# Performance work log

Hardware: AMD Instinct MI355X
Metric: run time of the kernel (lower is better)

## Reference

```python
import jax, jax.numpy as jnp
import numpy as np

EPS_BN = 1e-5
EPS_COS = 1e-8

N, F_IN, HID, OUT, S, NNZ = 50000, 1024, 256, 280, 5000, 800000


def setup_inputs() -> dict:
    key = jax.random.key(0)
    ks = jax.random.split(key, 20)
    inp = {}
    inp["x"] = jax.random.normal(ks[0], (N, F_IN), jnp.float32)
    inp["y"] = jax.random.normal(ks[1], (S, OUT), jnp.float32)
    inp["adj_rows"] = jax.random.randint(ks[2], (NNZ,), 0, N, jnp.int32)
    inp["adj_cols"] = jax.random.randint(ks[3], (NNZ,), 0, N, jnp.int32)
    inp["adj_vals"] = jax.random.uniform(ks[4], (NNZ,), jnp.float32)
    inp["agg_rows"] = jax.random.randint(ks[5], (N,), 0, S, jnp.int32)
    inp["agg_vals"] = jax.random.uniform(ks[6], (N,), jnp.float32)
    inp["perm"] = jax.random.permutation(ks[7], N).astype(jnp.int32)
    # parameters (kaiming-ish scale)
    def lin(k, fi, fo):
        k1, k2 = jax.random.split(k)
        w = jax.random.normal(k1, (fi, fo), jnp.float32) / np.sqrt(fi)
        b = jax.random.normal(k2, (fo,), jnp.float32) * 0.01
        return w, b
    inp["mlp_W"], inp["mlp_b"] = lin(ks[8], F_IN, HID)
    inp["bn_gamma"] = jnp.ones((HID,), jnp.float32)
    inp["bn_beta"] = jnp.zeros((HID,), jnp.float32)
    inp["hg_W1"], inp["hg_b1"] = lin(ks[9], HID, HID)
    inp["hg_W2"], inp["hg_b2"] = lin(ks[10], HID, HID)
    inp["hg_prelu"] = jnp.float32(0.25)
    inp["pred_W"], inp["pred_b"] = lin(ks[11], HID, OUT)
    inp["dgi_W"], inp["dgi_b"] = lin(ks[12], HID, OUT)
    inp["dgi_prelu"] = jnp.float32(0.25)
    return inp


def _spmm(rows, cols, vals, M, n_out):
    # sparse(H) @ M : gather source rows, scale by edge value, scatter-add to dest
    return jax.ops.segment_sum(vals[:, None] * M[cols], rows, num_segments=n_out)


def _prelu(t, a):
    return jnp.where(t >= 0, t, a * t)


def _leaky(t, s):
    return jnp.where(t >= 0, t, s * t)


def reference(x, y, adj_rows, adj_cols, adj_vals, agg_rows, agg_vals, perm,
              mlp_W, mlp_b, bn_gamma, bn_beta, hg_W1, hg_b1, hg_W2, hg_b2,
              hg_prelu, pred_W, pred_b, dgi_W, dgi_b, dgi_prelu):
    n = x.shape[0]
    s = y.shape[0]
    # mlp: Linear -> LeakyReLU(0.1) -> BatchNorm1d (batch stats, training mode)
    h0 = _leaky(x @ mlp_W + mlp_b, 0.1)
    mu = jnp.mean(h0, axis=0)
    var = jnp.mean((h0 - mu) ** 2, axis=0)  # biased, as torch BN training
    h0 = bn_gamma * (h0 - mu) * jax.lax.rsqrt(var + EPS_BN) + bn_beta
    # HGNN, num_layers=2 (dropout = identity in eval)
    t = _spmm(adj_rows, adj_cols, adj_vals, h0 @ hg_W1 + hg_b1, n)
    t = _prelu(t, hg_prelu)
    t = _spmm(adj_rows, adj_cols, adj_vals, t @ hg_W2 + hg_b2, n)
    h = _leaky(t, 0.01)
    x_prime = _leaky(h @ pred_W + pred_b, 0.01)
    # Xenium: loss = MSE(agg_mtx @ x_prime, y); agg_mtx has one nnz per cell
    agg = jax.ops.segment_sum(agg_vals[:, None] * x_prime, agg_rows, num_segments=s)
    loss = jnp.mean((agg - y) ** 2)
    # DGI (1-layer HGNN with PReLU)
    h1 = _prelu(_spmm(adj_rows, adj_cols, adj_vals, h0 @ dgi_W + dgi_b, n), dgi_prelu)
    c = jnp.mean(h1, axis=0)  # (OUT,)
    h2 = _prelu(_spmm(adj_rows, adj_cols, adj_vals, h0[perm] @ dgi_W + dgi_b, n), dgi_prelu)
    c_norm = jnp.linalg.norm(c)
    def cos(hm):
        return (hm @ c) / jnp.maximum(jnp.linalg.norm(hm, axis=1) * c_norm, EPS_COS)
    loss = loss + jnp.mean(1.0 - cos(h1)) + jnp.mean(jnp.maximum(cos(h2), 0.0))
    return (loss, x_prime)
```

## Files before the change

kernel.cpp:

```cpp
#include <hip/hip_runtime.h>
#include <hip/hip_bf16.h>

#define DEVI __device__ __forceinline__

typedef __attribute__((ext_vector_type(8))) short short8;
typedef __attribute__((ext_vector_type(4))) float float4v;

DEVI float bf2f(__hip_bfloat16 v) { return __bfloat162float(v); }
DEVI float ldbs(const ushort* p, size_t i) { return bf2f(((const __hip_bfloat16*)p)[i]); }
DEVI ushort f2bs(float v) {
    __hip_bfloat16 h = __float2bfloat16(v);
    return *(ushort*)&h;
}
DEVI float bfs2f(short s) {
    ushort u = (ushort)s;
    return bf2f(*(__hip_bfloat16*)&u);
}

DEVI float ldin(const void* p, size_t i, int isf32) {
    return isf32 ? ((const float*)p)[i] : bf2f(((const __hip_bfloat16*)p)[i]);
}
DEVI void stio(void* p, size_t i, float v, int isf32) {
    if (isf32) ((float*)p)[i] = v;
    else ((ushort*)p)[i] = f2bs(v);
}

template <int ACT>
DEVI float act_fn(float v, float alpha) {
    if (ACT == 1) return v >= 0.f ? v : 0.1f * v;
    if (ACT == 2) return v >= 0.f ? v : 0.01f * v;
    if (ACT == 3) return v >= 0.f ? v : alpha * v;
    return v;
}

DEVI float waveRed(float v) {
#pragma unroll
    for (int o = 32; o > 0; o >>= 1) v += __shfl_down(v, o);
    return v;
}

DEVI float blockRed(float v) {
    __shared__ float sm[16];
    int lane = threadIdx.x & 63, w = threadIdx.x >> 6;
    v = waveRed(v);
    if (lane == 0) sm[w] = v;
    __syncthreads();
    if (w == 0) {
        int nw = (blockDim.x + 63) >> 6;
        v = (lane < nw) ? sm[lane] : 0.f;
        v = waveRed(v);
    }
    return v;
}

__global__ void probe_k(const void* __restrict__ x, int* __restrict__ flag) {
    __shared__ int sfails;
    int t = threadIdx.x;
    if (t == 0) sfails = 0;
    __syncthreads();
    const __hip_bfloat16* xb = (const __hip_bfloat16*)x;
    int my = 0;
    for (int i = t; i < 4096; i += 256) {
        float v = bf2f(xb[i]);
        float a = fabsf(v);
        if (!(a <= 64.f) || (v != 0.f && a < 1e-6f)) my++;
    }
    atomicAdd(&sfails, my);
    __syncthreads();
    if (t == 0) flag[0] = (sfails > 409) ? 1 : 0;
}

struct Cvt5 {
    const void* src[5];
    ushort* dst[5];
    int K[5];
    int N[5];
};
__global__ void cvt_all_k(Cvt5 d, const int* __restrict__ flagp) {
    int f32 = flagp[0];
    int seg = blockIdx.y;
    int idx = blockIdx.x * blockDim.x + threadIdx.x;
    int K = d.K[seg], Nc = d.N[seg];
    int total = K * Nc;
    if (idx < total) {
        int k = idx / Nc, n = idx % Nc;
        d.dst[seg][(size_t)n * K + k] = f2bs(ldin(d.src[seg], idx, f32));
    }
}

#define TP 40
template <int AMODE, int ACT, int OMODE, int BMODE>
__global__ __launch_bounds__(256) void mgemm_k(
    const void* __restrict__ A, const ushort* __restrict__ Bt,
    const void* __restrict__ bias, const float* __restrict__ rsc,
    const void* __restrict__ alpha_p, void* __restrict__ outp, ushort* __restrict__ outp2,
    const int* __restrict__ flagp, int M, int K, int Nc, int LDo) {
    __shared__ short As[128 * TP];
    __shared__ short Bs[128 * TP];
    const int f32 = flagp[0];
    const int tid = threadIdx.x;
    const int lane = tid & 63;
    const int l15 = lane & 15;
    const int quad = lane >> 4;
    const int wid = tid >> 6;
    const int mW = (wid >> 1) * 64;
    const int nW = (wid & 1) * 64;
    const int mBase = blockIdx.y * 128;
    const int nBase = blockIdx.x * 128;

    float4v acc[4][4];
#pragma unroll
    for (int i = 0; i < 4; i++)
#pragma unroll
        for (int j = 0; j < 4; j++) acc[i][j] = (float4v){0.f, 0.f, 0.f, 0.f};

    short8 sa[2], sb[2];
    float4v fa[2][2];

    auto issue_tile = [&](int k0) {
#pragma unroll
        for (int i = 0; i < 2; i++) {
            int chunk = i * 256 + tid;
            int row = chunk >> 2;
            int c = chunk & 3;
            int gr = mBase + row;
            int gn = nBase + row;
            size_t geA = (size_t)gr * K + k0 + c * 8;
            if (AMODE == 0 && f32) {
                if (gr < M) {
                    const float* af = (const float*)A + geA;
                    fa[i][0] = *(const float4v*)af;
                    fa[i][1] = *(const float4v*)(af + 4);
                } else {
                    fa[i][0] = (float4v){0.f, 0.f, 0.f, 0.f};
                    fa[i][1] = (float4v){0.f, 0.f, 0.f, 0.f};
                }
            } else {
                sa[i] = (gr < M) ? *(const short8*)((const ushort*)A + geA)
                                 : (short8){0, 0, 0, 0, 0, 0, 0, 0};
            }
            sb[i] = (gn < Nc) ? *(const short8*)(Bt + (size_t)gn * K + k0 + c * 8)
                              : (short8){0, 0, 0, 0, 0, 0, 0, 0};
        }
    };

    auto commit_tile = [&]() {
#pragma unroll
        for (int i = 0; i < 2; i++) {
            int chunk = i * 256 + tid;
            int row = chunk >> 2;
            int c = chunk & 3;
            short8 va;
            if (AMODE == 0 && f32) {
#pragma unroll
                for (int j = 0; j < 4; j++) va[j] = (short)f2bs(fa[i][0][j]);
#pragma unroll
                for (int j = 0; j < 4; j++) va[4 + j] = (short)f2bs(fa[i][1][j]);
            } else {
                va = sa[i];
            }
            *(short8*)&As[row * TP + c * 8] = va;
            *(short8*)&Bs[row * TP + c * 8] = sb[i];
        }
    };

    const int nk = K >> 5;
    issue_tile(0);
    for (int t = 0; t < nk; ++t) {
        __syncthreads();
        commit_tile();
        if (t + 1 < nk) issue_tile((t + 1) << 5);
        __syncthreads();

        short8 af[4], bf[4];
#pragma unroll
        for (int i = 0; i < 4; i++)
            af[i] = *(const short8*)&As[(mW + i * 16 + l15) * TP + quad * 8];
#pragma unroll
        for (int j = 0; j < 4; j++)
            bf[j] = *(const short8*)&Bs[(nW + j * 16 + l15) * TP + quad * 8];
#pragma unroll
        for (int i = 0; i < 4; i++)
#pragma unroll
            for (int j = 0; j < 4; j++)
                acc[i][j] =
                    __builtin_amdgcn_mfma_f32_16x16x32_bf16(af[i], bf[j], acc[i][j], 0, 0, 0);
    }

    const float alpha = (ACT == 3) ? ldin(alpha_p, 0, f32) : 0.f;
#pragma unroll
    for (int i = 0; i < 4; i++) {
#pragma unroll
        for (int j = 0; j < 4; j++) {
            int gcn = nBase + nW + j * 16 + l15;
            if (gcn >= Nc) continue;
            float bv = ldin(bias, gcn, f32);
#pragma unroll
            for (int r = 0; r < 4; r++) {
                int grm = mBase + mW + i * 16 + quad * 4 + r;
                if (grm >= M) continue;
                float be = (BMODE == 1) ? rsc[grm] * bv : bv;
                float v = act_fn<ACT>(acc[i][j][r] + be, alpha);
                if (OMODE == 1) {
                    stio(outp, 1 + (size_t)grm * Nc + gcn, v, f32);
                    outp2[(size_t)grm * LDo + gcn] = f2bs(v);
                } else {
                    ((ushort*)outp)[(size_t)grm * LDo + gcn] = f2bs(v);
                }
            }
        }
    }
}

__global__ void count_k(const int* __restrict__ rows, int* __restrict__ counts, int nnz) {
    int i = blockIdx.x * blockDim.x + threadIdx.x;
    if (i < nnz) atomicAdd(&counts[rows[i]], 1);
}

__global__ __launch_bounds__(1024) void scan_local_k(const int* __restrict__ counts,
                                                     int* __restrict__ offs,
                                                     int* __restrict__ bsums, int n) {
    __shared__ int sm[1024];
    int t = threadIdx.x;
    int g = blockIdx.x * 1024 + t;
    int v = (g < n) ? counts[g] : 0;
    sm[t] = v;
    __syncthreads();
    for (int d = 1; d < 1024; d <<= 1) {
        int add = (t >= d) ? sm[t - d] : 0;
        __syncthreads();
        sm[t] += add;
        __syncthreads();
    }
    if (g < n) offs[g] = sm[t] - v;
    if (t == 1023) bsums[blockIdx.x] = sm[t];
}

__global__ void scan_bsums_k(int* bsums, int nb) {
    if (threadIdx.x == 0 && blockIdx.x == 0) {
        int acc = 0;
        for (int i = 0; i < nb; i++) {
            int v = bsums[i];
            bsums[i] = acc;
            acc += v;
        }
    }
}

__global__ void scan_add_k(int* __restrict__ offs, const int* __restrict__ bsums, int n, int nnz) {
    int g = blockIdx.x * blockDim.x + threadIdx.x;
    if (g < n) offs[g] += bsums[g >> 10];
    if (g == 0) offs[n] = nnz;
}

__global__ void fill_k(const int* __restrict__ rows, const int* __restrict__ cols,
                       const void* __restrict__ vals, const int* __restrict__ perm,
                       const int* __restrict__ offs, int* __restrict__ cursor,
                       int* __restrict__ cols_s, int* __restrict__ colsp_s,
                       float* __restrict__ vals_s, float* __restrict__ rsum,
                       const int* __restrict__ flagp, int nnz) {
    int e = blockIdx.x * blockDim.x + threadIdx.x;
    if (e < nnz) {
        int r = rows[e];
        int pos = offs[r] + atomicAdd(&cursor[r], 1);
        int c = cols[e];
        float v = ldin(vals, e, flagp[0]);
        cols_s[pos] = c;
        colsp_s[pos] = perm[c];
        vals_s[pos] = v;
        atomicAdd(&rsum[r], v);
    }
}

__global__ void fill_s_k(const int* __restrict__ rows, const void* __restrict__ vals,
                         const int* __restrict__ offs, int* __restrict__ cursor,
                         int* __restrict__ idx_s, float* __restrict__ val_s,
                         const int* __restrict__ flagp, int n) {
    int e = blockIdx.x * blockDim.x + threadIdx.x;
    if (e < n) {
        int r = rows[e];
        int pos = offs[r] + atomicAdd(&cursor[r], 1);
        idx_s[pos] = e;
        val_s[pos] = ldin(vals, e, flagp[0]);
    }
}

template <int ACT, bool DUAL>
__global__ __launch_bounds__(256) void spmms_k(
    const int* __restrict__ offs, const int* __restrict__ cols_s,
    const int* __restrict__ colsp_s, const float* __restrict__ vals_s,
    const void* __restrict__ alpha_p, const int* __restrict__ flagp,
    const ushort* __restrict__ Min, ushort* __restrict__ out1, ushort* __restrict__ out2,
    int Nrow, int LD) {
    int bid = blockIdx.x;
    int slice = bid & 7;
    int row = (bid >> 3) * 4 + (threadIdx.x >> 6);
    if (row >= Nrow) return;
    int lane = threadIdx.x & 63;
    int e = lane >> 2, ch = lane & 3;
    int sbase = slice * 32 + ch * 8;
    float alpha = (ACT == 3) ? ldin(alpha_p, 0, flagp[0]) : 0.f;
    int s = offs[row], en = offs[row + 1];
    float a[8] = {}, b[8] = {};
    for (int i = s + e; i < en; i += 16) {
        int c = cols_s[i];
        float v = vals_s[i];
        short8 h = *(const short8*)(Min + (size_t)c * LD + sbase);
#pragma unroll
        for (int j = 0; j < 8; j++) a[j] += v * bfs2f(h[j]);
        if (DUAL) {
            int cp = colsp_s[i];
            short8 g = *(const short8*)(Min + (size_t)cp * LD + sbase);
#pragma unroll
            for (int j = 0; j < 8; j++) b[j] += v * bfs2f(g[j]);
        }
    }
#pragma unroll
    for (int m = 4; m < 64; m <<= 1) {
#pragma unroll
        for (int j = 0; j < 8; j++) {
            a[j] += __shfl_xor(a[j], m);
            if (DUAL) b[j] += __shfl_xor(b[j], m);
        }
    }
    if (e == 0) {
        short8 o;
        size_t obase = (size_t)row * LD + sbase;
#pragma unroll
        for (int j = 0; j < 8; j++) o[j] = (short)f2bs(act_fn<ACT>(a[j], alpha));
        *(short8*)(out1 + obase) = o;
        if (DUAL) {
#pragma unroll
            for (int j = 0; j < 8; j++) o[j] = (short)f2bs(act_fn<ACT>(b[j], alpha));
            *(short8*)(out2 + obase) = o;
        }
    }
}

__global__ __launch_bounds__(256) void aggmse_k(
    const int* __restrict__ soffs, const int* __restrict__ sidx, const float* __restrict__ sval,
    const ushort* __restrict__ xp, const void* __restrict__ y, const int* __restrict__ flagp,
    float* __restrict__ lacc, int S, int F, int LDxp) {
    int srow = blockIdx.x * 4 + (threadIdx.x >> 6);
    int lane = threadIdx.x & 63;
    int half = lane >> 5, l5 = lane & 31;
    int FC = F >> 3;
    bool has1 = (l5 + 32) < FC;
    float a0[8] = {}, a1[8] = {};
    if (srow < S) {
        int s = soffs[srow], e = soffs[srow + 1];
        constexpr int DEPTH = 4;
        int i = s + half;
        for (; i + 2 * (DEPTH - 1) < e; i += 2 * DEPTH) {
            int n[DEPTH];
            float v[DEPTH];
#pragma unroll
            for (int u = 0; u < DEPTH; u++) {
                n[u] = sidx[i + 2 * u];
                v[u] = sval[i + 2 * u];
            }
            short8 h0v[DEPTH], h1v[DEPTH];
#pragma unroll
            for (int u = 0; u < DEPTH; u++) {
                const ushort* src = xp + (size_t)n[u] * LDxp;
                h0v[u] = *(const short8*)(src + l5 * 8);
                if (has1) h1v[u] = *(const short8*)(src + (l5 + 32) * 8);
            }
#pragma unroll
            for (int u = 0; u < DEPTH; u++) {
#pragma unroll
                for (int j = 0; j < 8; j++) a0[j] += v[u] * bfs2f(h0v[u][j]);
                if (has1) {
#pragma unroll
                    for (int j = 0; j < 8; j++) a1[j] += v[u] * bfs2f(h1v[u][j]);
                }
            }
        }
        for (; i < e; i += 2) {
            float v = sval[i];
            int n = sidx[i];
            const ushort* src = xp + (size_t)n * LDxp;
            short8 h = *(const short8*)(src + l5 * 8);
#pragma unroll
            for (int j = 0; j < 8; j++) a0[j] += v * bfs2f(h[j]);
            if (has1) {
                short8 h2 = *(const short8*)(src + (l5 + 32) * 8);
#pragma unroll
                for (int j = 0; j < 8; j++) a1[j] += v * bfs2f(h2[j]);
            }
        }
    }
#pragma unroll
    for (int j = 0; j < 8; j++) {
        a0[j] += __shfl_xor(a0[j], 32);
        if (has1) a1[j] += __shfl_xor(a1[j], 32);
    }
    float ss = 0.f;
    if (srow < S && half == 0) {
        int f32 = flagp[0];
        size_t base = (size_t)srow * F;
#pragma unroll
        for (int j = 0; j < 8; j++) {
            float d = a0[j] - ldin(y, base + l5 * 8 + j, f32);
            ss += d * d;
        }
        if (has1) {
#pragma unroll
            for (int j = 0; j < 8; j++) {
                float d = a1[j] - ldin(y, base + (l5 + 32) * 8 + j, f32);
                ss += d * d;
            }
        }
    }
    ss = blockRed(ss);
    if (threadIdx.x == 0) atomicAdd(&lacc[0], ss);
}

__global__ __launch_bounds__(256) void bn_stats_k(const ushort* __restrict__ h,
                                                  float* __restrict__ sum,
                                                  float* __restrict__ sumsq, int nrows, int rpb) {
    int c = threadIdx.x;
    int rs = blockIdx.x * rpb;
    int re = min(rs + rpb, nrows);
    float s = 0.f, s2 = 0.f;
    int H = blockDim.x;
    for (int r = rs; r < re; r++) {
        float v = ldbs(h, (size_t)r * H + c);
        s += v;
        s2 += v * v;
    }
    atomicAdd(&sum[c], s);
    atomicAdd(&sumsq[c], s2);
}

__global__ void bn_final_k(const float* __restrict__ sum, const float* __restrict__ sumsq,
                           const void* __restrict__ gamma, const void* __restrict__ beta,
                           float* __restrict__ scale, float* __restrict__ shift,
                           const int* __restrict__ flagp, int nrows) {
    int c = threadIdx.x;
    int f32 = flagp[0];
    float mu = sum[c] / nrows;
    float var = sumsq[c] / nrows - mu * mu;
    float sc = ldin(gamma, c, f32) * rsqrtf(var + 1e-5f);
    scale[c] = sc;
    shift[c] = ldin(beta, c, f32) - mu * sc;
}

__global__ __launch_bounds__(256) void bn_apply_k(ushort* __restrict__ h,
                                                  const float* __restrict__ scale,
                                                  const float* __restrict__ shift, int total8,
                                                  int H) {
    int idx = blockIdx.x * 256 + threadIdx.x;
    if (idx >= total8) return;
    size_t base = (size_t)idx * 8;
    int c = (int)(base % H);
    short8 v = *(short8*)(h + base);
    short8 o;
#pragma unroll
    for (int j = 0; j < 8; j++) o[j] = (short)f2bs(bfs2f(v[j]) * scale[c + j] + shift[c + j]);
    *(short8*)(h + base) = o;
}

__global__ __launch_bounds__(320) void colsum_k(const ushort* __restrict__ h,
                                                float* __restrict__ accum, int nrows, int F,
                                                int rpb) {
    int f = threadIdx.x;
    if (f >= F) return;
    int rs = blockIdx.x * rpb;
    int re = min(rs + rpb, nrows);
    float s = 0.f;
    for (int r = rs; r < re; r++) s += ldbs(h, (size_t)r * F + f);
    atomicAdd(&accum[f], s);
}

__global__ __launch_bounds__(320) void cfinal_k(const float* __restrict__ accum,
                                                float* __restrict__ c, float* __restrict__ cnorm,
                                                int N, int F) {
    int f = threadIdx.x;
    float v = 0.f;
    if (f < F) {
        v = accum[f] / N;
        c[f] = v;
    }
    float s2 = blockRed(v * v);
    if (threadIdx.x == 0) cnorm[0] = sqrtf(s2);
}

template <int MODE>
__global__ __launch_bounds__(256) void cos_k(const ushort* __restrict__ h,
                                             const float* __restrict__ c,
                                             const float* __restrict__ cnorm,
                                             float* __restrict__ acc, int N, int F) {
    int gw = (blockIdx.x * blockDim.x + threadIdx.x) >> 6;
    int lane = threadIdx.x & 63;
    int nw = (gridDim.x * blockDim.x) >> 6;
    float cn = cnorm[0];
    float s = 0.f;
    for (int row = gw; row < N; row += nw) {
        float dot = 0.f, nsq = 0.f;
        for (int f = lane; f < F; f += 64) {
            float v = ldbs(h, (size_t)row * F + f);
            dot += v * c[f];
            nsq += v * v;
        }
#pragma unroll
        for (int o = 32; o > 0; o >>= 1) {
            dot += __shfl_down(dot, o);
            nsq += __shfl_down(nsq, o);
        }
        if (lane == 0) {
            float cosv = dot / fmaxf(sqrtf(nsq) * cn, 1e-8f);
            s += (MODE == 1) ? fmaxf(cosv, 0.f) : cosv;
        }
    }
    s = blockRed(s);
    if (threadIdx.x == 0) atomicAdd(acc, s);
}

__global__ void final_k(const float* __restrict__ lacc, void* __restrict__ dout,
                        const int* __restrict__ flagp, int SOUT, int N) {
    if (threadIdx.x == 0 && blockIdx.x == 0) {
        float loss = lacc[0] / SOUT + (1.f - lacc[1] / N) + lacc[2] / N;
        stio(dout, 0, loss, flagp[0]);
    }
}

extern "C" void kernel_launch(void* const* d_in, const int* in_sizes, int n_in,
                              void* d_out, int out_size, void* d_ws, size_t ws_size,
                              hipStream_t stream) {
    const void* x = d_in[0];
    const void* y = d_in[1];
    const int* adj_rows = (const int*)d_in[2];
    const int* adj_cols = (const int*)d_in[3];
    const void* adj_vals = d_in[4];
    const int* agg_rows = (const int*)d_in[5];
    const void* agg_vals = d_in[6];
    const int* perm = (const int*)d_in[7];
    const void* mlp_W = d_in[8];
    const void* mlp_b = d_in[9];
    const void* bn_gamma = d_in[10];
    const void* bn_beta = d_in[11];
    const void* hg_W1 = d_in[12];
    const void* hg_b1 = d_in[13];
    const void* hg_W2 = d_in[14];
    const void* hg_b2 = d_in[15];
    const void* hg_prelu = d_in[16];
    const void* pred_W = d_in[17];
    const void* pred_b = d_in[18];
    const void* dgi_W = d_in[19];
    const void* dgi_b = d_in[20];
    const void* dgi_prelu = d_in[21];

    const int N = in_sizes[5];
    const int NNZ = in_sizes[2];
    const int F_IN = in_sizes[0] / N;
    const int HID = in_sizes[9];
    const int OUT = in_sizes[18];
    const int S = in_sizes[1] / OUT;

    const int LDP = (OUT + 63) & ~63;

    char* w = (char*)d_ws;
    size_t off = 0;
    auto alloc = [&](size_t b) -> char* {
        char* p = w + off;
        off += (b + 255) & ~(size_t)255;
        return p;
    };
    ushort* h0_bf = (ushort*)alloc((size_t)N * HID * 2);
    ushort* U_bf = (ushort*)alloc((size_t)N * HID * 2);
    ushort* Up_bf = (ushort*)alloc((size_t)N * HID * 2);
    ushort* zA_bf = (ushort*)alloc((size_t)N * LDP * 2);
    ushort* zB_bf = (ushort*)alloc((size_t)N * LDP * 2);
    ushort* h2_bf = (ushort*)alloc((size_t)N * OUT * 2);
    ushort* xp_ws = zA_bf;
    ushort* mlpWt = (ushort*)alloc((size_t)HID * F_IN * 2);
    ushort* hgW1t = (ushort*)alloc((size_t)HID * HID * 2);
    ushort* hgW2t = (ushort*)alloc((size_t)HID * HID * 2);
    ushort* predWt = (ushort*)alloc((size_t)OUT * HID * 2);
    ushort* dgiWt = (ushort*)alloc((size_t)OUT * HID * 2);
    int* offs = (int*)alloc((size_t)(N + 1) * 4);
    int nbscan = (N + 1023) / 1024;
    int* bsums = (int*)alloc((size_t)nbscan * 4);
    int* cols_s = (int*)alloc((size_t)NNZ * 4);
    int* colsp_s = (int*)alloc((size_t)NNZ * 4);
    float* vals_s = (float*)alloc((size_t)NNZ * 4);
    int* soffs = (int*)alloc((size_t)(S + 1) * 4);
    int nbscan_s = (S + 1023) / 1024;
    int* sbsums = (int*)alloc((size_t)nbscan_s * 4);
    int* sidx = (int*)alloc((size_t)N * 4);
    float* sval = (float*)alloc((size_t)N * 4);
    float* bn_scale = (float*)alloc((size_t)HID * 4);
    float* bn_shift = (float*)alloc((size_t)HID * 4);
    float* c_vec = (float*)alloc((size_t)OUT * 4);
    float* cnorm = (float*)alloc(4);
    int* dflag = (int*)alloc(16);
    char* zero_base = w + off;
    int* counts = (int*)alloc((size_t)N * 4);
    int* cursor = (int*)alloc((size_t)N * 4);
    int* scnt = (int*)alloc((size_t)S * 4);
    int* scursor = (int*)alloc((size_t)S * 4);
    float* rsum = (float*)alloc((size_t)N * 4);
    float* bn_sum = (float*)alloc((size_t)HID * 4);
    float* bn_sumsq = (float*)alloc((size_t)HID * 4);
    float* c_acc = (float*)alloc((size_t)OUT * 4);
    float* lacc = (float*)alloc(16);
    size_t zero_bytes = (w + off) - zero_base;
    hipMemsetAsync(zero_base, 0, zero_bytes, stream);

    probe_k<<<1, 256, 0, stream>>>(x, dflag);

    Cvt5 cv;
    cv.src[0] = mlp_W;  cv.dst[0] = mlpWt;  cv.K[0] = F_IN; cv.N[0] = HID;
    cv.src[1] = hg_W1;  cv.dst[1] = hgW1t;  cv.K[1] = HID;  cv.N[1] = HID;
    cv.src[2] = hg_W2;  cv.dst[2] = hgW2t;  cv.K[2] = HID;  cv.N[2] = HID;
    cv.src[3] = pred_W; cv.dst[3] = predWt; cv.K[3] = HID;  cv.N[3] = OUT;
    cv.src[4] = dgi_W;  cv.dst[4] = dgiWt;  cv.K[4] = HID;  cv.N[4] = OUT;
    cvt_all_k<<<dim3((F_IN * HID + 255) / 256, 5), 256, 0, stream>>>(cv, dflag);

    count_k<<<(NNZ + 255) / 256, 256, 0, stream>>>(adj_rows, counts, NNZ);
    scan_local_k<<<nbscan, 1024, 0, stream>>>(counts, offs, bsums, N);
    scan_bsums_k<<<1, 64, 0, stream>>>(bsums, nbscan);
    scan_add_k<<<(N + 255) / 256, 256, 0, stream>>>(offs, bsums, N, NNZ);
    fill_k<<<(NNZ + 255) / 256, 256, 0, stream>>>(adj_rows, adj_cols, adj_vals, perm, offs,
                                                  cursor, cols_s, colsp_s, vals_s, rsum, dflag,
                                                  NNZ);
    count_k<<<(N + 255) / 256, 256, 0, stream>>>(agg_rows, scnt, N);
    scan_local_k<<<nbscan_s, 1024, 0, stream>>>(scnt, soffs, sbsums, S);
    scan_bsums_k<<<1, 64, 0, stream>>>(sbsums, nbscan_s);
    scan_add_k<<<(S + 255) / 256, 256, 0, stream>>>(soffs, sbsums, S, N);
    fill_s_k<<<(N + 255) / 256, 256, 0, stream>>>(agg_rows, agg_vals, soffs, scursor, sidx, sval,
                                                  dflag, N);

    const int MT = (N + 127) / 128;
    const int NT_H = (HID + 127) / 128;
    const int NT_O = (OUT + 127) / 128;
    const int SGRID = ((N + 3) / 4) * 8;

    mgemm_k<0, 1, 0, 0><<<dim3(NT_H, MT), 256, 0, stream>>>(
        x, mlpWt, mlp_b, nullptr, nullptr, h0_bf, nullptr, dflag, N, F_IN, HID, HID);
    bn_stats_k<<<(N + 127) / 128, HID, 0, stream>>>(h0_bf, bn_sum, bn_sumsq, N, 128);
    bn_final_k<<<1, HID, 0, stream>>>(bn_sum, bn_sumsq, bn_gamma, bn_beta, bn_scale, bn_shift,
                                      dflag, N);
    {
        int total8 = (N * HID) / 8;
        bn_apply_k<<<(total8 + 255) / 256, 256, 0, stream>>>(h0_bf, bn_scale, bn_shift, total8,
                                                             HID);
    }

    spmms_k<0, true><<<SGRID, 256, 0, stream>>>(offs, cols_s, colsp_s, vals_s, nullptr, dflag,
                                                h0_bf, U_bf, Up_bf, N, HID);

    mgemm_k<1, 3, 0, 1><<<dim3(NT_H, MT), 256, 0, stream>>>(
        U_bf, hgW1t, hg_b1, rsum, hg_prelu, zB_bf, nullptr, dflag, N, HID, HID, HID);
    mgemm_k<1, 0, 0, 0><<<dim3(NT_H, MT), 256, 0, stream>>>(
        zB_bf, hgW2t, hg_b2, nullptr, nullptr, zA_bf, nullptr, dflag, N, HID, HID, HID);
    spmms_k<2, false><<<SGRID, 256, 0, stream>>>(offs, cols_s, nullptr, vals_s, nullptr, dflag,
                                                 zA_bf, zB_bf, nullptr, N, HID);

    mgemm_k<1, 2, 1, 0><<<dim3(NT_O, MT), 256, 0, stream>>>(
        zB_bf, predWt, pred_b, nullptr, nullptr, d_out, xp_ws, dflag, N, HID, OUT, LDP);
    aggmse_k<<<(S + 3) / 4, 256, 0, stream>>>(soffs, sidx, sval, xp_ws, y, dflag, lacc, S, OUT,
                                              LDP);

    mgemm_k<1, 3, 0, 1><<<dim3(NT_O, MT), 256, 0, stream>>>(
        U_bf, dgiWt, dgi_b, rsum, dgi_prelu, zB_bf, nullptr, dflag, N, HID, OUT, OUT);
    mgemm_k<1, 3, 0, 1><<<dim3(NT_O, MT), 256, 0, stream>>>(
        Up_bf, dgiWt, dgi_b, rsum, dgi_prelu, h2_bf, nullptr, dflag, N, HID, OUT, OUT);

    colsum_k<<<(N + 127) / 128, 320, 0, stream>>>(zB_bf, c_acc, N, OUT, 128);
    cfinal_k<<<1, 320, 0, stream>>>(c_acc, c_vec, cnorm, N, OUT);
    cos_k<0><<<256, 256, 0, stream>>>(zB_bf, c_vec, cnorm, &lacc[1], N, OUT);
    cos_k<1><<<256, 256, 0, stream>>>(h2_bf, c_vec, cnorm, &lacc[2], N, OUT);

    final_k<<<1, 64, 0, stream>>>(lacc, d_out, dflag, S * OUT, N);
}
```

Before: 1.488 ms.

## Fold BatchNorm apply into first SpMM epilogue and restructure SpMM row mapping

Removes the separate BatchNorm apply pass over h0 and instead applies scale and shift algebraically in the first SpMM epilogue (scale*acc + rowsum*shift), relying on the linearity of the sparse aggregation. The SpMM kernel is also restructured so each wavefront covers a full 256-wide row (two halves of 32 lanes splitting the edges) with a depth-4 software-prefetched gather loop, instead of 8 column-slice blocks per row with 16-way edge splitting. This saves one full read and write of h0 and reduces the shuffle reduction, but h0 is now stored pre-normalisation in bf16, which changes rounding. LD is hardcoded to 256.

```diff
diff --git a/kernel.cpp b/kernel.cpp
--- a/kernel.cpp
+++ b/kernel.cpp
@@ -285,26 +285,58 @@
     }
 }
 
-template <int ACT, bool DUAL>
-__global__ __launch_bounds__(256) void spmms_k(
+template <int ACT, bool DUAL, int EPI>
+__global__ __launch_bounds__(256) void spmmv_k(
     const int* __restrict__ offs, const int* __restrict__ cols_s,
     const int* __restrict__ colsp_s, const float* __restrict__ vals_s,
     const void* __restrict__ alpha_p, const int* __restrict__ flagp,
     const ushort* __restrict__ Min, ushort* __restrict__ out1, ushort* __restrict__ out2,
-    int Nrow, int LD) {
-    int bid = blockIdx.x;
-    int slice = bid & 7;
-    int row = (bid >> 3) * 4 + (threadIdx.x >> 6);
+    const float* __restrict__ scale, const float* __restrict__ shift,
+    const float* __restrict__ rsum, int Nrow) {
+    const int LD = 256;
+    int row = blockIdx.x * 4 + (threadIdx.x >> 6);
     if (row >= Nrow) return;
     int lane = threadIdx.x & 63;
-    int e = lane >> 2, ch = lane & 3;
-    int sbase = slice * 32 + ch * 8;
+    int half = lane >> 5, l5 = lane & 31;
+    int sbase = l5 * 8;
     float alpha = (ACT == 3) ? ldin(alpha_p, 0, flagp[0]) : 0.f;
-    int s = offs[row], en = offs[row + 1];
+    int s = offs[row], e = offs[row + 1];
     float a[8] = {}, b[8] = {};
-    for (int i = s + e; i < en; i += 16) {
+
+    constexpr int DEPTH = 4;
+    int i = s + half;
+    for (; i + 2 * (DEPTH - 1) < e; i += 2 * DEPTH) {
+        int c[DEPTH];
+        float v[DEPTH];
+        int cp[DEPTH];
+#pragma unroll
+        for (int u = 0; u < DEPTH; u++) {
+            c[u] = cols_s[i + 2 * u];
+            v[u] = vals_s[i + 2 * u];
+        }
+        if (DUAL) {
+#pragma unroll
+            for (int u = 0; u < DEPTH; u++) cp[u] = colsp_s[i + 2 * u];
+        }
+        short8 hv[DEPTH], gv[DEPTH];
+#pragma unroll
+        for (int u = 0; u < DEPTH; u++) {
+            hv[u] = *(const short8*)(Min + (size_t)c[u] * LD + sbase);
+            if (DUAL) gv[u] = *(const short8*)(Min + (size_t)cp[u] * LD + sbase);
+        }
+#pragma unroll
+        for (int u = 0; u < DEPTH; u++) {
+#pragma unroll
+            for (int j = 0; j < 8; j++) a[j] += v[u] * bfs2f(hv[u][j]);
+            if (DUAL) {
+#pragma unroll
+                for (int j = 0; j < 8; j++) b[j] += v[u] * bfs2f(gv[u][j]);
+            }
+        }
+    }
+    for (; i < e; i += 2) {
+        float v = vals_s[i];
         int c = cols_s[i];
-        float v = vals_s[i];
         short8 h = *(const short8*)(Min + (size_t)c * LD + sbase);
 #pragma unroll
         for (int j = 0; j < 8; j++) a[j] += v * bfs2f(h[j]);
@@ -316,23 +348,41 @@
         }
     }
 #pragma unroll
-    for (int m = 4; m < 64; m <<= 1) {
-#pragma unroll
-        for (int j = 0; j < 8; j++) {
-            a[j] += __shfl_xor(a[j], m);
-            if (DUAL) b[j] += __shfl_xor(b[j], m);
-        }
-    }
-    if (e == 0) {
+    for (int j = 0; j < 8; j++) {
+        a[j] += __shfl_xor(a[j], 32);
+        if (DUAL) b[j] += __shfl_xor(b[j], 32);
+    }
+    if (half == 0) {
+        size_t obase = (size_t)row * LD + sbase;
         short8 o;
-        size_t obase = (size_t)row * LD + sbase;
-#pragma unroll
-        for (int j = 0; j < 8; j++) o[j] = (short)f2bs(act_fn<ACT>(a[j], alpha));
-        *(short8*)(out1 + obase) = o;
-        if (DUAL) {
-#pragma unroll
-            for (int j = 0; j < 8; j++) o[j] = (short)f2bs(act_fn<ACT>(b[j], alpha));
-            *(short8*)(out2 + obase) = o;
+        if (EPI == 1) {
+            float4v sc0 = *(const float4v*)(scale + sbase);
+            float4v sc1 = *(const float4v*)(scale + sbase + 4);
+            float4v sh0 = *(const float4v*)(shift + sbase);
+            float4v sh1 = *(const float4v*)(shift + sbase + 4);
+            float rr = rsum[row];
+#pragma unroll
+            for (int j = 0; j < 4; j++) o[j] = (short)f2bs(sc0[j] * a[j] + rr * sh0[j]);
+#pragma unroll
+            for (int j = 0; j < 4; j++) o[4 + j] = (short)f2bs(sc1[j] * a[4 + j] + rr * sh1[j]);
+            *(short8*)(out1 + obase) = o;
+            if (DUAL) {
+#pragma unroll
+                for (int j = 0; j < 4; j++) o[j] = (short)f2bs(sc0[j] * b[j] + rr * sh0[j]);
+#pragma unroll
+                for (int j = 0; j < 4; j++)
+                    o[4 + j] = (short)f2bs(sc1[j] * b[4 + j] + rr * sh1[j]);
+                *(short8*)(out2 + obase) = o;
+            }
+        } else {
+#pragma unroll
+            for (int j = 0; j < 8; j++) o[j] = (short)f2bs(act_fn<ACT>(a[j], alpha));
+            *(short8*)(out1 + obase) = o;
+            if (DUAL) {
+#pragma unroll
+                for (int j = 0; j < 8; j++) o[j] = (short)f2bs(act_fn<ACT>(b[j], alpha));
+                *(short8*)(out2 + obase) = o;
+            }
         }
     }
 }
@@ -444,21 +494,6 @@
     float sc = ldin(gamma, c, f32) * rsqrtf(var + 1e-5f);
     scale[c] = sc;
     shift[c] = ldin(beta, c, f32) - mu * sc;
-}
-
-__global__ __launch_bounds__(256) void bn_apply_k(ushort* __restrict__ h,
-                                                  const float* __restrict__ scale,
-                                                  const float* __restrict__ shift, int total8,
-                                                  int H) {
-    int idx = blockIdx.x * 256 + threadIdx.x;
-    if (idx >= total8) return;
-    size_t base = (size_t)idx * 8;
-    int c = (int)(base % H);
-    short8 v = *(short8*)(h + base);
-    short8 o;
-#pragma unroll
-    for (int j = 0; j < 8; j++) o[j] = (short)f2bs(bfs2f(v[j]) * scale[c + j] + shift[c + j]);
-    *(short8*)(h + base) = o;
 }
 
 __global__ __launch_bounds__(320) void colsum_k(const ushort* __restrict__ h,
@@ -635,28 +670,24 @@
     const int MT = (N + 127) / 128;
     const int NT_H = (HID + 127) / 128;
     const int NT_O = (OUT + 127) / 128;
-    const int SGRID = ((N + 3) / 4) * 8;
+    const int SPB = (N + 3) / 4;
 
     mgemm_k<0, 1, 0, 0><<<dim3(NT_H, MT), 256, 0, stream>>>(
         x, mlpWt, mlp_b, nullptr, nullptr, h0_bf, nullptr, dflag, N, F_IN, HID, HID);
     bn_stats_k<<<(N + 127) / 128, HID, 0, stream>>>(h0_bf, bn_sum, bn_sumsq, N, 128);
     bn_final_k<<<1, HID, 0, stream>>>(bn_sum, bn_sumsq, bn_gamma, bn_beta, bn_scale, bn_shift,
                                       dflag, N);
-    {
-        int total8 = (N * HID) / 8;
-        bn_apply_k<<<(total8 + 255) / 256, 256, 0, stream>>>(h0_bf, bn_scale, bn_shift, total8,
-                                                             HID);
-    }
-
-    spmms_k<0, true><<<SGRID, 256, 0, stream>>>(offs, cols_s, colsp_s, vals_s, nullptr, dflag,
-                                                h0_bf, U_bf, Up_bf, N, HID);
+
+    spmmv_k<0, true, 1><<<SPB, 256, 0, stream>>>(offs, cols_s, colsp_s, vals_s, nullptr, dflag,
+                                                 h0_bf, U_bf, Up_bf, bn_scale, bn_shift, rsum, N);
 
     mgemm_k<1, 3, 0, 1><<<dim3(NT_H, MT), 256, 0, stream>>>(
         U_bf, hgW1t, hg_b1, rsum, hg_prelu, zB_bf, nullptr, dflag, N, HID, HID, HID);
     mgemm_k<1, 0, 0, 0><<<dim3(NT_H, MT), 256, 0, stream>>>(
         zB_bf, hgW2t, hg_b2, nullptr, nullptr, zA_bf, nullptr, dflag, N, HID, HID, HID);
-    spmms_k<2, false><<<SGRID, 256, 0, stream>>>(offs, cols_s, nullptr, vals_s, nullptr, dflag,
-                                                 zA_bf, zB_bf, nullptr, N, HID);
+    spmmv_k<2, false, 0><<<SPB, 256, 0, stream>>>(offs, cols_s, nullptr, vals_s, nullptr, dflag,
+                                                  zA_bf, zB_bf, nullptr, nullptr, nullptr,
+                                                  nullptr, N);
 
     mgemm_k<1, 2, 1, 0><<<dim3(NT_O, MT), 256, 0, stream>>>(
         zB_bf, predWt, pred_b, nullptr, nullptr, d_out, xp_ws, dflag, N, HID, OUT, LDP);
```

Result: faster. 1.201 ms (-19.2%).
